# Kernel optimization log

Hardware: AMD Instinct MI355X
Metric: run time of the kernel (lower is better)

## Reference

```python
import jax, jax.numpy as jnp
import numpy as np

EPS = 1e-8       # epsilon added to abs-diff in compute_sim
LN_EPS = 1e-5    # torch nn.LayerNorm default eps
NUM_HEADS = 8


def _layernorm(x, g, b):
    mu = jnp.mean(x, axis=-1, keepdims=True)
    var = jnp.mean((x - mu) ** 2, axis=-1, keepdims=True)
    return (x - mu) / jnp.sqrt(var + LN_EPS) * g + b


def _fla(x, alphas, betas):
    # x: [B, D]; alphas/betas: [H, 3] scalars per (head, {query,key,value})
    D = x.shape[-1]
    scale = 1.0 / jnp.sqrt(jnp.float32(D))
    acc = jnp.zeros_like(x)
    for h in range(alphas.shape[0]):  # small fixed head count; avoids H*B*D*D blowup
        q = alphas[h, 0] * x + betas[h, 0]
        k = alphas[h, 1] * x + betas[h, 1]
        v = alphas[h, 2] * x + betas[h, 2]
        # sim[b,i,j] = 1/(|q[b,j]-k[b,i]|+eps), softmax over j, scaled by 1/sqrt(D)
        sim = jax.nn.softmax(1.0 / (jnp.abs(q[:, None, :] - k[:, :, None]) + EPS), axis=-1) * scale
        acc = acc + jnp.einsum('bij,bj->bi', sim, v)
    return x + acc


def setup_inputs() -> dict:
    key = jax.random.key(0)
    ks = jax.random.split(key, 8)
    B, D, L = 1024, 256, 2  # batch, feature dim (input_dim == hidden dims), num hidden layers
    x = jax.random.normal(ks[0], (B, D), dtype=jnp.float32)
    fla_alphas = jax.random.uniform(ks[1], (L, NUM_HEADS, 3), dtype=jnp.float32)
    fla_betas = jax.random.uniform(ks[2], (L, NUM_HEADS, 3), dtype=jnp.float32)
    lim = 1.0 / np.sqrt(D)
    lin_W = jax.random.uniform(ks[3], (L, D, D), dtype=jnp.float32, minval=-lim, maxval=lim)
    lin_b = jax.random.uniform(ks[4], (L, D), dtype=jnp.float32, minval=-lim, maxval=lim)
    fla_ln_g = jnp.ones((L, D), jnp.float32)
    fla_ln_b = jnp.zeros((L, D), jnp.float32)
    lin_ln_g = jnp.ones((L, D), jnp.float32)
    lin_ln_b = jnp.zeros((L, D), jnp.float32)
    out_W = jax.random.uniform(ks[5], (D, 1), dtype=jnp.float32, minval=-lim, maxval=lim)
    out_b = jax.random.uniform(ks[6], (1,), dtype=jnp.float32, minval=-lim, maxval=lim)
    return dict(x=x, fla_alphas=fla_alphas, fla_betas=fla_betas,
                fla_ln_g=fla_ln_g, fla_ln_b=fla_ln_b,
                lin_W=lin_W, lin_b=lin_b,
                lin_ln_g=lin_ln_g, lin_ln_b=lin_ln_b,
                out_W=out_W, out_b=out_b)


def reference(x, fla_alphas, fla_betas, fla_ln_g, fla_ln_b,
              lin_W, lin_b, lin_ln_g, lin_ln_b, out_W, out_b):
    L = fla_alphas.shape[0]
    for i in range(L):
        x = _fla(x, fla_alphas[i], fla_betas[i])
        x = jax.nn.relu(x)
        x = _layernorm(x, fla_ln_g[i], fla_ln_b[i])
        x = x @ lin_W[i] + lin_b[i]
        x = jax.nn.relu(x)
        x = _layernorm(x, lin_ln_g[i], lin_ln_b[i])
    return x @ out_W + out_b
```

## Files before the change

### kernel.cpp

```cpp
#include <hip/hip_runtime.h>

#define DD 256
#define NH 8
#define HPT 2
#define NHG 4

constexpr float LN_EPS = 1e-5f;
constexpr float SCALE  = 0.0625f;
constexpr float KS     = 8.2629579e-8f;
constexpr float B_EXP  = 1064986816.0f;
constexpr float T0     = 2.0625e8f;
#define RCP_MAGIC 0x7EF311C3u

__device__ __forceinline__ float wexp_clamped(float dh, float Bh) {
    float y = __uint_as_float(RCP_MAGIC - __float_as_uint(dh));
    float w = fmaf(-fabsf(dh), fabsf(y), 2.0f);
    float f = fminf(fmaf(fabsf(y), w, Bh), B_EXP);
    unsigned u;
    asm("v_cvt_u32_f32 %0, %1" : "=v"(u) : "v"(f));
    return __uint_as_float(u);
}

__device__ __forceinline__ int lb256(const float* __restrict__ a, float t) {
    int p = 0;
    #pragma unroll
    for (int st = 128; st > 0; st >>= 1)
        p += (a[p + st - 1] < t) ? st : 0;
    return p;
}

__device__ __forceinline__ float2 fla_dense(const float4* __restrict__ xr4,
                                            float aqk, float ck, float Bh) {
    float sE0=0.f,sE1=0.f,sE2=0.f,sE3=0.f,sW0=0.f,sW1=0.f,sW2=0.f,sW3=0.f;
    #pragma unroll 2
    for (int j4 = 0; j4 < DD/4; ++j4) {
        float4 xj = xr4[j4];
        float e0 = wexp_clamped(fmaf(aqk, xj.x, ck), Bh);
        float e1 = wexp_clamped(fmaf(aqk, xj.y, ck), Bh);
        float e2 = wexp_clamped(fmaf(aqk, xj.z, ck), Bh);
        float e3 = wexp_clamped(fmaf(aqk, xj.w, ck), Bh);
        sE0 += e0; sW0 = fmaf(e0, xj.x, sW0);
        sE1 += e1; sW1 = fmaf(e1, xj.y, sW1);
        sE2 += e2; sW2 = fmaf(e2, xj.z, sW2);
        sE3 += e3; sW3 = fmaf(e3, xj.w, sW3);
    }
    return make_float2((sE0+sE1)+(sE2+sE3), (sW0+sW1)+(sW2+sW3));
}

__device__ __forceinline__ float2 fla_head(const float* __restrict__ xsrt,
                                           const float4* __restrict__ xr4,
                                           float aqk, float ck) {
    float inv_aqk = __builtin_amdgcn_rcpf(aqk);
    float xstar = fminf(fmaxf(-ck * inv_aqk, -1e5f), 1e5f);
    int pos = lb256(xsrt, xstar);
    pos += (xsrt[pos] < xstar) ? 1 : 0;
    int i1 = (pos - 1 > 0) ? pos - 1 : 0;
    int i2 = (pos < DD - 1) ? pos : DD - 1;
    float d1 = fabsf(fmaf(aqk, xsrt[i1], ck));
    float d2 = fabsf(fmaf(aqk, xsrt[i2], ck));
    float dm = fminf(d1, d2);
    float ym = __uint_as_float(RCP_MAGIC - __float_as_uint(dm));
    float m  = fabsf(ym) * fmaf(-dm, fabsf(ym), 2.0f);
    float Bh = B_EXP - m;
    float mm = fmaf(m, 0.9375f, -T0);
    if (__all(mm > 0.f)) {
        float halfw = __builtin_amdgcn_rcpf(mm) * fabsf(inv_aqk);
        float vlo = xstar - halfw, vhi = xstar + halfw;
        int lo = lb256(xsrt, vlo); lo = (lo < i1) ? lo : i1;
        int hi = lb256(xsrt, vhi); hi += (xsrt[hi] < vhi) ? 1 : 0;
        hi = (hi > i2 + 1) ? hi : i2 + 1;
        float sE = 0.f, sW = 0.f;
        for (int idx = lo; idx < hi; ++idx) {
            float xsv = xsrt[idx];
            float e = wexp_clamped(fmaf(aqk, xsv, ck), Bh);
            sE += e; sW = fmaf(e, xsv, sW);
        }
        return make_float2(sE, sW);
    }
    return fla_dense(xr4, aqk, ck, Bh);
}

__device__ __forceinline__ float2 block_reduce2(float a, float b, float* sc, int tid) {
    #pragma unroll
    for (int off = 32; off; off >>= 1) {
        a += __shfl_down(a, off, 64);
        b += __shfl_down(b, off, 64);
    }
    __syncthreads();
    if ((tid & 63) == 0) { int w = tid >> 6; sc[w] = a; sc[16 + w] = b; }
    __syncthreads();
    const float4* s4 = reinterpret_cast<const float4*>(sc);
    float4 a0 = s4[0], a1 = s4[1], a2 = s4[2], a3 = s4[3];
    float4 b0 = s4[4], b1 = s4[5], b2 = s4[6], b3 = s4[7];
    float ra = ((a0.x+a0.y)+(a0.z+a0.w)) + ((a1.x+a1.y)+(a1.z+a1.w))
             + ((a2.x+a2.y)+(a2.z+a2.w)) + ((a3.x+a3.y)+(a3.z+a3.w));
    float rb = ((b0.x+b0.y)+(b0.z+b0.w)) + ((b1.x+b1.y)+(b1.z+b1.w))
             + ((b2.x+b2.y)+(b2.z+b2.w)) + ((b3.x+b3.y)+(b3.z+b3.w));
    return make_float2(ra, rb);
}

template<int LAST>
__global__ __launch_bounds__(1024, 8) void flann_layer(
    const float* __restrict__ x_in,
    const float* __restrict__ alphas,
    const float* __restrict__ betas,
    const float* __restrict__ g1, const float* __restrict__ b1,
    const float* __restrict__ W,  const float* __restrict__ wb,
    const float* __restrict__ g2, const float* __restrict__ b2,
    const float* __restrict__ outW, const float* __restrict__ outB,
    float* __restrict__ out)
{
    __shared__ __align__(16) float xsrt[DD];
    __shared__ __align__(16) float xln[DD];
    __shared__ float comb[NHG][DD];
    __shared__ float sc[32];

    const int tid  = threadIdx.x;
    const int i    = tid & (DD - 1);
    const int hg   = tid >> 8;
    const int bidx = blockIdx.x;

    const float*  xrow = x_in + bidx * DD;
    const float4* xr4  = reinterpret_cast<const float4*>(xrow);
    float xv = xrow[i];

    {
        float v = xv;
        float* flat = &comb[0][0];
        #pragma unroll
        for (int k = 2; k <= DD; k <<= 1) {
            #pragma unroll
            for (int j = k >> 1; j > 0; j >>= 1) {
                float p;
                if (j < 64) {
                    p = __shfl_xor(v, j, 64);
                } else {
                    flat[tid] = v;
                    __syncthreads();
                    p = flat[tid ^ j];
                    __syncthreads();
                }
                bool keepmin = (((i & j) == 0) == ((i & k) == 0));
                v = keepmin ? fminf(v, p) : fmaxf(v, p);
            }
        }
        if (hg == 0) xsrt[i] = v;
        __syncthreads();
    }

    const int h0 = hg * HPT;
    const float aq0 = alphas[h0*3+0], ak0 = alphas[h0*3+1], av0 = alphas[h0*3+2];
    const float bq0 = betas [h0*3+0], bk0 = betas [h0*3+1], bv0 = betas [h0*3+2];
    const float aq1 = alphas[h0*3+3], ak1 = alphas[h0*3+4], av1 = alphas[h0*3+5];
    const float bq1 = betas [h0*3+3], bk1 = betas [h0*3+4], bv1 = betas [h0*3+5];
    const float aqk0 = aq0 * KS, aqk1 = aq1 * KS;
    const float ck0  = (bq0 - fmaf(ak0, xv, bk0)) * KS;
    const float ck1  = (bq1 - fmaf(ak1, xv, bk1)) * KS;

    float2 s0 = fla_head(xsrt, xr4, aqk0, ck0);
    float2 s1 = fla_head(xsrt, xr4, aqk1, ck1);

    float yE0 = __uint_as_float(RCP_MAGIC - __float_as_uint(s0.x));
    float rE0 = fabsf(yE0) * fmaf(-s0.x, fabsf(yE0), 2.0f);
    rE0 = rE0 * fmaf(-s0.x, rE0, 2.0f);
    float yE1 = __uint_as_float(RCP_MAGIC - __float_as_uint(s1.x));
    float rE1 = fabsf(yE1) * fmaf(-s1.x, fabsf(yE1), 2.0f);
    rE1 = rE1 * fmaf(-s1.x, rE1, 2.0f);
    float accp = fmaf(av0, s0.y, bv0 * s0.x) * rE0
               + fmaf(av1, s1.y, bv1 * s1.x) * rE1;
    comb[hg][i] = accp;
    __syncthreads();

    float xr = 0.f;
    if (hg == 0) {
        float acc = (comb[0][i] + comb[1][i]) + (comb[2][i] + comb[3][i]);
        xr = fmaxf(fmaf(SCALE, acc, xv), 0.f);
    }

    float2 r = block_reduce2(xr, xr * xr, sc, tid);
    float mu  = r.x * (1.f / DD);
    float var = r.y * (1.f / DD) - mu * mu;
    if (hg == 0) {
        float xn = (xr - mu) * __builtin_amdgcn_rsqf(var + LN_EPS);
        xln[i] = fmaf(xn, g1[i], b1[i]);
    }
    __syncthreads();

    const float4* xl4 = reinterpret_cast<const float4*>(xln);
    float ga0 = (hg == 0) ? wb[i] : 0.f, ga1 = 0.f, ga2 = 0.f, ga3 = 0.f;
    #pragma unroll 4
    for (int d4 = 0; d4 < DD/16; ++d4) {
        int g4 = hg * (DD/16) + d4;
        float4 xd = xl4[g4];
        int dr = 4 * g4;
        ga0 = fmaf(xd.x, W[(dr + 0) * DD + i], ga0);
        ga1 = fmaf(xd.y, W[(dr + 1) * DD + i], ga1);
        ga2 = fmaf(xd.z, W[(dr + 2) * DD + i], ga2);
        ga3 = fmaf(xd.w, W[(dr + 3) * DD + i], ga3);
    }
    comb[hg][i] = (ga0 + ga1) + (ga2 + ga3);
    __syncthreads();

    float gv = 0.f;
    if (hg == 0)
        gv = fmaxf((comb[0][i] + comb[1][i]) + (comb[2][i] + comb[3][i]), 0.f);

    r = block_reduce2(gv, gv * gv, sc, tid);
    mu  = r.x * (1.f / DD);
    var = r.y * (1.f / DD) - mu * mu;
    float xo = 0.f;
    if (hg == 0)
        xo = fmaf((gv - mu) * __builtin_amdgcn_rsqf(var + LN_EPS), g2[i], b2[i]);

    if (!LAST) {
        if (hg == 0) out[bidx * DD + i] = xo;
    } else {
        float pr = (hg == 0) ? xo * outW[i] : 0.f;
        float2 p = block_reduce2(pr, 0.f, sc, tid);
        if (tid == 0) out[bidx] = p.x + outB[0];
    }
}

extern "C" void kernel_launch(void* const* d_in, const int* in_sizes, int n_in,
                              void* d_out, int out_size, void* d_ws, size_t ws_size,
                              hipStream_t stream) {
    const float* x      = (const float*)d_in[0];
    const float* alphas = (const float*)d_in[1];
    const float* betas  = (const float*)d_in[2];
    const float* flag   = (const float*)d_in[3];
    const float* flab   = (const float*)d_in[4];
    const float* linW   = (const float*)d_in[5];
    const float* linb   = (const float*)d_in[6];
    const float* ling   = (const float*)d_in[7];
    const float* linb2  = (const float*)d_in[8];
    const float* outW   = (const float*)d_in[9];
    const float* outB   = (const float*)d_in[10];

    const int B = in_sizes[0] / DD;
    float* ws   = (float*)d_ws;
    float* outp = (float*)d_out;

    dim3 grid(B), block(1024);
    flann_layer<0><<<grid, block, 0, stream>>>(
        x, alphas, betas, flag, flab, linW, linb, ling, linb2,
        nullptr, nullptr, ws);
    flann_layer<1><<<grid, block, 0, stream>>>(
        ws, alphas + NH*3, betas + NH*3, flag + DD, flab + DD,
        linW + DD*DD, linb + DD, ling + DD, linb2 + DD,
        outW, outB, outp);
}
```

Baseline: 161.2 us.

## Replace windowed/dense split with outward float4 scan over sorted row

```diff
diff --git a/kernel.cpp b/kernel.cpp
--- a/kernel.cpp
+++ b/kernel.cpp
@@ -9,7 +9,7 @@
 constexpr float SCALE  = 0.0625f;
 constexpr float KS     = 8.2629579e-8f;
 constexpr float B_EXP  = 1064986816.0f;
-constexpr float T0     = 2.0625e8f;
+constexpr float T0     = 1.36150e8f;
 #define RCP_MAGIC 0x7EF311C3u
 
 __device__ __forceinline__ float wexp_clamped(float dh, float Bh) {
@@ -29,12 +29,33 @@
     return p;
 }
 
-__device__ __forceinline__ float2 fla_dense(const float4* __restrict__ xr4,
-                                            float aqk, float ck, float Bh) {
-    float sE0=0.f,sE1=0.f,sE2=0.f,sE3=0.f,sW0=0.f,sW1=0.f,sW2=0.f,sW3=0.f;
-    #pragma unroll 2
-    for (int j4 = 0; j4 < DD/4; ++j4) {
-        float4 xj = xr4[j4];
+__device__ __forceinline__ float2 fla_head(const float* __restrict__ xsrt,
+                                           float aqk, float ck) {
+    float inv_aqk = __builtin_amdgcn_rcpf(aqk);
+    float xstar = fminf(fmaxf(-ck * inv_aqk, -1e5f), 1e5f);
+    int pos = lb256(xsrt, xstar);
+    pos += (xsrt[pos] < xstar) ? 1 : 0;
+    int i1 = (pos - 1 > 0) ? pos - 1 : 0;
+    int i2 = (pos < DD - 1) ? pos : DD - 1;
+    float x2 = xsrt[i2];
+    float d1 = fabsf(fmaf(aqk, xsrt[i1], ck));
+    float d2 = fabsf(fmaf(aqk, x2, ck));
+    float dm = fminf(d1, d2);
+    float ym = __uint_as_float(RCP_MAGIC - __float_as_uint(dm));
+    float m  = fabsf(ym) * fmaf(-dm, fabsf(ym), 2.0f);
+    float Bh = B_EXP - m;
+    float mm = fmaf(m, 0.9375f, -T0);
+    float halfw = (mm > 0.f) ? __builtin_amdgcn_rcpf(mm) * fabsf(inv_aqk)
+                             : 3e38f;
+    float vlo = xstar - halfw;
+    float vhi = fmaxf(xstar + halfw, x2);
+
+    const float4* xs4 = reinterpret_cast<const float4*>(xsrt);
+    float sE0=0.f,sE1=0.f,sE2=0.f,sE3=0.f;
+    float sW0=0.f,sW1=0.f,sW2=0.f,sW3=0.f;
+    const int c0 = i1 >> 2;
+    for (int ci = c0; ci >= 0; --ci) {
+        float4 xj = xs4[ci];
         float e0 = wexp_clamped(fmaf(aqk, xj.x, ck), Bh);
         float e1 = wexp_clamped(fmaf(aqk, xj.y, ck), Bh);
         float e2 = wexp_clamped(fmaf(aqk, xj.z, ck), Bh);
@@ -43,41 +64,21 @@
         sE1 += e1; sW1 = fmaf(e1, xj.y, sW1);
         sE2 += e2; sW2 = fmaf(e2, xj.z, sW2);
         sE3 += e3; sW3 = fmaf(e3, xj.w, sW3);
+        if (xj.x < vlo) break;
+    }
+    for (int ci = c0 + 1; ci < DD/4; ++ci) {
+        float4 xj = xs4[ci];
+        if (xj.x > vhi) break;
+        float e0 = wexp_clamped(fmaf(aqk, xj.x, ck), Bh);
+        float e1 = wexp_clamped(fmaf(aqk, xj.y, ck), Bh);
+        float e2 = wexp_clamped(fmaf(aqk, xj.z, ck), Bh);
+        float e3 = wexp_clamped(fmaf(aqk, xj.w, ck), Bh);
+        sE0 += e0; sW0 = fmaf(e0, xj.x, sW0);
+        sE1 += e1; sW1 = fmaf(e1, xj.y, sW1);
+        sE2 += e2; sW2 = fmaf(e2, xj.z, sW2);
+        sE3 += e3; sW3 = fmaf(e3, xj.w, sW3);
     }
     return make_float2((sE0+sE1)+(sE2+sE3), (sW0+sW1)+(sW2+sW3));
-}
-
-__device__ __forceinline__ float2 fla_head(const float* __restrict__ xsrt,
-                                           const float4* __restrict__ xr4,
-                                           float aqk, float ck) {
-    float inv_aqk = __builtin_amdgcn_rcpf(aqk);
-    float xstar = fminf(fmaxf(-ck * inv_aqk, -1e5f), 1e5f);
-    int pos = lb256(xsrt, xstar);
-    pos += (xsrt[pos] < xstar) ? 1 : 0;
-    int i1 = (pos - 1 > 0) ? pos - 1 : 0;
-    int i2 = (pos < DD - 1) ? pos : DD - 1;
-    float d1 = fabsf(fmaf(aqk, xsrt[i1], ck));
-    float d2 = fabsf(fmaf(aqk, xsrt[i2], ck));
-    float dm = fminf(d1, d2);
-    float ym = __uint_as_float(RCP_MAGIC - __float_as_uint(dm));
-    float m  = fabsf(ym) * fmaf(-dm, fabsf(ym), 2.0f);
-    float Bh = B_EXP - m;
-    float mm = fmaf(m, 0.9375f, -T0);
-    if (__all(mm > 0.f)) {
-        float halfw = __builtin_amdgcn_rcpf(mm) * fabsf(inv_aqk);
-        float vlo = xstar - halfw, vhi = xstar + halfw;
-        int lo = lb256(xsrt, vlo); lo = (lo < i1) ? lo : i1;
-        int hi = lb256(xsrt, vhi); hi += (xsrt[hi] < vhi) ? 1 : 0;
-        hi = (hi > i2 + 1) ? hi : i2 + 1;
-        float sE = 0.f, sW = 0.f;
-        for (int idx = lo; idx < hi; ++idx) {
-            float xsv = xsrt[idx];
-            float e = wexp_clamped(fmaf(aqk, xsv, ck), Bh);
-            sE += e; sW = fmaf(e, xsv, sW);
-        }
-        return make_float2(sE, sW);
-    }
-    return fla_dense(xr4, aqk, ck, Bh);
 }
 
 __device__ __forceinline__ float2 block_reduce2(float a, float b, float* sc, int tid) {
@@ -120,8 +121,7 @@
     const int hg   = tid >> 8;
     const int bidx = blockIdx.x;
 
-    const float*  xrow = x_in + bidx * DD;
-    const float4* xr4  = reinterpret_cast<const float4*>(xrow);
+    const float* xrow = x_in + bidx * DD;
     float xv = xrow[i];
 
     {
@@ -157,8 +157,8 @@
     const float ck0  = (bq0 - fmaf(ak0, xv, bk0)) * KS;
     const float ck1  = (bq1 - fmaf(ak1, xv, bk1)) * KS;
 
-    float2 s0 = fla_head(xsrt, xr4, aqk0, ck0);
-    float2 s1 = fla_head(xsrt, xr4, aqk1, ck1);
+    float2 s0 = fla_head(xsrt, aqk0, ck0);
+    float2 s1 = fla_head(xsrt, aqk1, ck1);
 
     float yE0 = __uint_as_float(RCP_MAGIC - __float_as_uint(s0.x));
     float rE0 = fabsf(yE0) * fmaf(-s0.x, fabsf(yE0), 2.0f);
```

Measured after the change: 224.5 us. 39.3% more time.
